# Optimization experiments

Measured on AMD Instinct MI355X. Metric: run time of the kernel, lower is better.

Reference implementation:

```python
import jax, jax.numpy as jnp
import numpy as np

IN_DIM = 128
OUT_DIM = 128
N_NODES = 50000
N_EDGES = 800000


def setup_inputs() -> dict:
    key = jax.random.key(0)
    ks = jax.random.split(key, 8)
    x = jax.random.normal(ks[0], (N_NODES, IN_DIM), dtype=jnp.float32)
    edge_index = jax.random.randint(ks[1], (2, N_EDGES), 0, N_NODES, dtype=jnp.int64)
    # SAGEConv params (PyG): lin_l applied to aggregated neighbors (has bias),
    # lin_r applied to root features (no bias).
    s = 1.0 / np.sqrt(IN_DIM)
    W_l = jax.random.uniform(ks[2], (IN_DIM, OUT_DIM), jnp.float32, -s, s)
    b_l = jax.random.uniform(ks[3], (OUT_DIM,), jnp.float32, -s, s)
    W_r = jax.random.uniform(ks[4], (IN_DIM, OUT_DIM), jnp.float32, -s, s)
    gamma = jnp.ones((OUT_DIM,), jnp.float32)
    beta = jnp.zeros((OUT_DIM,), jnp.float32)
    return {"x": x, "edge_index": edge_index, "W_l": W_l, "b_l": b_l,
            "W_r": W_r, "gamma": gamma, "beta": beta}


def reference(x, edge_index, W_l, b_l, W_r, gamma, beta):
    src, dst = edge_index[0], edge_index[1]
    # mean aggregation of source features at target nodes
    msg_sum = jax.ops.segment_sum(x[src], dst, num_segments=N_NODES)  # [N, in]
    cnt = jax.ops.segment_sum(jnp.ones((N_EDGES,), x.dtype), dst, num_segments=N_NODES)
    agg = msg_sum / jnp.maximum(cnt, 1.0)[:, None]
    # SAGEConv: lin_l(agg) + lin_r(x)
    out = agg @ W_l + b_l + x @ W_r  # [N, out]
    # LayerNorm over feature dim (eps=1e-5, torch default)
    mu = jnp.mean(out, axis=-1, keepdims=True)
    var = jnp.mean(jnp.square(out - mu), axis=-1, keepdims=True)
    out = (out - mu) * jax.lax.rsqrt(var + 1e-5) * gamma + beta
    # ReLU; dropout is identity in eval mode
    return jax.nn.relu(out)
```

## Files before the change

kernel.cpp:

```cpp
#include <hip/hip_runtime.h>

#define N_NODES 50000
#define N_EDGES 800000
#define DIM 128
#define M_PAD 50048

#define BNODES 64
#define NBUCK 782
#define SLACK 1280
#define EPB   4096
#define NBLKA ((N_EDGES + EPB - 1) / EPB)
#define SPLIT 2

#define M_TILE 32
#define MW 2

typedef __attribute__((ext_vector_type(8))) short bf16x8;
typedef __attribute__((ext_vector_type(4))) float f32x4;

#define WS_BUF_OFF 4096
#define WS_XH_OFF  (WS_BUF_OFF + (size_t)NBUCK * SLACK * 4)
#define WS_WT_OFF  (WS_XH_OFF + (size_t)M_PAD * DIM * 2)

static __device__ __forceinline__ unsigned short f2b(float f) {
    unsigned int x = __float_as_uint(f);
    x += 0x7fffu + ((x >> 16) & 1u);
    return (unsigned short)(x >> 16);
}
static __device__ __forceinline__ float blo(unsigned int v) {
    return __uint_as_float(v << 16);
}
static __device__ __forceinline__ float bhi(unsigned int v) {
    return __uint_as_float(v & 0xffff0000u);
}

#define CAST_BLOCKS 6250
#define WT_BLOCKS 64

__global__ __launch_bounds__(256) void prepA_kernel(
    const float* __restrict__ x,
    const float* __restrict__ Wl,
    const float* __restrict__ Wr,
    const int* __restrict__ src,
    const int* __restrict__ dst,
    unsigned short* __restrict__ xh,
    unsigned short* __restrict__ WhT,
    int* __restrict__ gcur,
    unsigned int* __restrict__ buf)
{
    __shared__ unsigned int img[EPB];
    __shared__ int hist[NBUCK];
    __shared__ int lbase[NBUCK];
    __shared__ int gbase[NBUCK];

    const int blk = blockIdx.x;
    const int tid = threadIdx.x;

    if (blk >= NBLKA) {
        int b = blk - NBLKA;
        if (b < CAST_BLOCKS) {
            int i = b * 256 + tid;
            float4 v = reinterpret_cast<const float4*>(x)[i];
            ushort4 h;
            h.x = f2b(v.x); h.y = f2b(v.y); h.z = f2b(v.z); h.w = f2b(v.w);
            reinterpret_cast<ushort4*>(xh)[i] = h;
        } else {
            int idx = (b - CAST_BLOCKS) * 256 + tid;
            int n = idx & 127;
            int k = idx >> 7;
            WhT[n * 256 + k]       = f2b(Wl[idx]);
            WhT[n * 256 + 128 + k] = f2b(Wr[idx]);
        }
        return;
    }

    const int e0 = blk * EPB;
    const int n = min(EPB, N_EDGES - e0);

    for (int i = tid; i < NBUCK; i += 256) hist[i] = 0;
    __syncthreads();
    for (int i = tid; i < n; i += 256)
        atomicAdd(&hist[dst[e0 + i] >> 6], 1);
    __syncthreads();
    if (tid < 64) {
        int c0 = tid * 13;
        int v[13];
        int s = 0;
        #pragma unroll
        for (int j = 0; j < 13; ++j) {
            int idx = c0 + j;
            v[j] = (idx < NBUCK) ? hist[idx] : 0;
            s += v[j];
        }
        int incl = s;
        #pragma unroll
        for (int d = 1; d < 64; d <<= 1) {
            int t = __shfl_up(incl, d, 64);
            if (tid >= d) incl += t;
        }
        int run = incl - s;
        #pragma unroll
        for (int j = 0; j < 13; ++j) {
            int idx = c0 + j;
            if (idx < NBUCK) lbase[idx] = run;
            run += v[j];
        }
    }
    __syncthreads();
    for (int i = tid; i < NBUCK; i += 256) {
        int c = hist[i];
        gbase[i] = i * SLACK + (c ? atomicAdd(&gcur[i], c) : 0);
        hist[i] = 0;
    }
    __syncthreads();
    for (int i = tid; i < n; i += 256) {
        int d = dst[e0 + i];
        int s = src[e0 + i];
        int b = d >> 6;
        int r = atomicAdd(&hist[b], 1);
        img[lbase[b] + r] = (unsigned int)s | ((unsigned int)d << 16);
    }
    __syncthreads();
    for (int i = tid; i < n; i += 256) {
        unsigned int v = img[i];
        int b = (int)(v >> 16) >> 6;
        int pos = gbase[b] + (i - lbase[b]);
        if (pos < (b + 1) * SLACK) buf[pos] = v;
    }
}

__global__ __launch_bounds__(256) void binBC_kernel(
    const unsigned int* __restrict__ buf,
    const int* __restrict__ gcur,
    const unsigned short* __restrict__ xh,
    const unsigned short* __restrict__ WhT,
    const float* __restrict__ bl,
    const float* __restrict__ gamma,
    const float* __restrict__ beta,
    float* __restrict__ out)
{
    __shared__ unsigned int ebuf[SLACK];
    __shared__ unsigned short csr[SLACK + 16];
    __shared__ int dhist[BNODES];
    __shared__ int dbase[BNODES];
    __shared__ int dcur[BNODES];
    __shared__ unsigned short aggh[M_TILE][DIM + 8];
    __shared__ float sRed[M_TILE][4][2];

    const int tid = threadIdx.x;
    const int w = tid >> 6;
    const int lane = tid & 63;
    const int r16 = lane & 15;
    const int kg = lane >> 4;
    const int b = blockIdx.x / SPLIT;
    const int half = blockIdx.x % SPLIT;
    const int rb = blockIdx.x * M_TILE;
    const int cnt = min(gcur[b], SLACK);
    const unsigned int* bp = buf + (size_t)b * SLACK;

    if (tid < BNODES) { dhist[tid] = 0; dcur[tid] = 0; }
    for (int i = tid; i < (SLACK + 16) / 2; i += 256)
        reinterpret_cast<unsigned int*>(csr)[i] = 0;
    for (int i = tid; i < cnt; i += 256) ebuf[i] = bp[i];
    __syncthreads();
    for (int i = tid; i < cnt; i += 256)
        atomicAdd(&dhist[(ebuf[i] >> 16) & 63], 1);
    __syncthreads();
    if (tid < 64) {
        int v = dhist[tid];
        int incl = v;
        #pragma unroll
        for (int d = 1; d < 64; d <<= 1) {
            int t = __shfl_up(incl, d, 64);
            if (tid >= d) incl += t;
        }
        dbase[tid] = incl - v;
    }
    __syncthreads();
    for (int i = tid; i < cnt; i += 256) {
        unsigned int v = ebuf[i];
        int d = (v >> 16) & 63;
        int r = atomicAdd(&dcur[d], 1);
        csr[dbase[d] + r] = (unsigned short)(v & 0xFFFFu);
    }
    __syncthreads();

    const unsigned int* xp = reinterpret_cast<const unsigned int*>(xh);
    for (int j = 0; j < M_TILE / 8; ++j) {
        int lnlA = w + 8 * j;
        int lnlB = lnlA + 4;
        int lnA = half * M_TILE + lnlA;
        int lnB = half * M_TILE + lnlB;
        int nodeA = b * BNODES + lnA;
        int nodeB = b * BNODES + lnB;
        int degA = (nodeA < N_NODES) ? dhist[lnA] : 0;
        int degB = (nodeB < N_NODES) ? dhist[lnB] : 0;
        int stA = dbase[lnA], stB = dbase[lnB];
        int dmA = max(degA - 1, 0), dmB = max(degB - 1, 0);
        float axA = 0.f, ayA = 0.f, axB = 0.f, ayB = 0.f;

        unsigned int vA[16], vB[16];
        #pragma unroll
        for (int t = 0; t < 16; ++t)
            vA[t] = xp[csr[stA + min(t, dmA)] * 64 + lane];
        #pragma unroll
        for (int t = 0; t < 16; ++t)
            vB[t] = xp[csr[stB + min(t, dmB)] * 64 + lane];
        #pragma unroll
        for (int t = 0; t < 16; ++t) {
            if (t < degA) { axA += blo(vA[t]); ayA += bhi(vA[t]); }
            if (t < degB) { axB += blo(vB[t]); ayB += bhi(vB[t]); }
        }
        for (int base = 16; base < degA; base += 8) {
            unsigned int u[8];
            #pragma unroll
            for (int t = 0; t < 8; ++t)
                u[t] = xp[csr[stA + min(base + t, dmA)] * 64 + lane];
            #pragma unroll
            for (int t = 0; t < 8; ++t)
                if (base + t < degA) { axA += blo(u[t]); ayA += bhi(u[t]); }
        }
        for (int base = 16; base < degB; base += 8) {
            unsigned int u[8];
            #pragma unroll
            for (int t = 0; t < 8; ++t)
                u[t] = xp[csr[stB + min(base + t, dmB)] * 64 + lane];
            #pragma unroll
            for (int t = 0; t < 8; ++t)
                if (base + t < degB) { axB += blo(u[t]); ayB += bhi(u[t]); }
        }
        float invA = 1.0f / (float)max(degA, 1);
        float invB = 1.0f / (float)max(degB, 1);
        unsigned int pkA = (unsigned int)f2b(axA * invA)
                         | ((unsigned int)f2b(ayA * invA) << 16);
        unsigned int pkB = (unsigned int)f2b(axB * invB)
                         | ((unsigned int)f2b(ayB * invB) << 16);
        *reinterpret_cast<unsigned int*>(&aggh[lnlA][lane * 2]) = pkA;
        *reinterpret_cast<unsigned int*>(&aggh[lnlB][lane * 2]) = pkB;
    }
    __syncthreads();

    f32x4 acc[MW][2];
    #pragma unroll
    for (int m = 0; m < MW; ++m)
        #pragma unroll
        for (int f = 0; f < 2; ++f)
            acc[m][f] = (f32x4){0.f, 0.f, 0.f, 0.f};

    #pragma unroll
    for (int kf = 0; kf < 8; ++kf) {
        bf16x8 a[MW];
        bf16x8 bfk[2];
        #pragma unroll
        for (int f = 0; f < 2; ++f)
            bfk[f] = *reinterpret_cast<const bf16x8*>(
                WhT + (w * 32 + f * 16 + r16) * 256 + kf * 32 + kg * 8);
        if (kf < 4) {
            #pragma unroll
            for (int m = 0; m < MW; ++m)
                a[m] = *reinterpret_cast<const bf16x8*>(
                    &aggh[m * 16 + r16][kf * 32 + kg * 8]);
        } else {
            #pragma unroll
            for (int m = 0; m < MW; ++m)
                a[m] = *reinterpret_cast<const bf16x8*>(
                    xh + (size_t)(rb + m * 16 + r16) * DIM + (kf - 4) * 32 + kg * 8);
        }
        #pragma unroll
        for (int m = 0; m < MW; ++m)
            #pragma unroll
            for (int f = 0; f < 2; ++f)
                acc[m][f] = __builtin_amdgcn_mfma_f32_16x16x32_bf16(
                    a[m], bfk[f], acc[m][f], 0, 0, 0);
    }

    float blv[2], gav[2], bev[2];
    #pragma unroll
    for (int f = 0; f < 2; ++f) {
        int col = w * 32 + f * 16 + r16;
        blv[f] = bl[col]; gav[f] = gamma[col]; bev[f] = beta[col];
    }
    #pragma unroll
    for (int m = 0; m < MW; ++m)
        #pragma unroll
        for (int r = 0; r < 4; ++r) {
            float v0 = acc[m][0][r] + blv[0];
            float v1 = acc[m][1][r] + blv[1];
            acc[m][0][r] = v0; acc[m][1][r] = v1;
            float s = v0 + v1;
            float q = v0 * v0 + v1 * v1;
            #pragma unroll
            for (int d = 1; d < 16; d <<= 1) {
                s += __shfl_xor(s, d, 16);
                q += __shfl_xor(q, d, 16);
            }
            if (r16 == 0) {
                sRed[m * 16 + kg * 4 + r][w][0] = s;
                sRed[m * 16 + kg * 4 + r][w][1] = q;
            }
        }
    __syncthreads();

    #pragma unroll
    for (int m = 0; m < MW; ++m)
        #pragma unroll
        for (int r = 0; r < 4; ++r) {
            int lr = m * 16 + kg * 4 + r;
            float S = sRed[lr][0][0] + sRed[lr][1][0] + sRed[lr][2][0] + sRed[lr][3][0];
            float Q = sRed[lr][0][1] + sRed[lr][1][1] + sRed[lr][2][1] + sRed[lr][3][1];
            float mean = S * (1.0f / 128.0f);
            float var = Q * (1.0f / 128.0f) - mean * mean;
            float rstd = rsqrtf(var + 1e-5f);
            int row = rb + lr;
            if (row < N_NODES) {
                #pragma unroll
                for (int f = 0; f < 2; ++f) {
                    float o = (acc[m][f][r] - mean) * rstd * gav[f] + bev[f];
                    out[(size_t)row * DIM + w * 32 + f * 16 + r16] = fmaxf(o, 0.f);
                }
            }
        }
}

extern "C" void kernel_launch(void* const* d_in, const int* in_sizes, int n_in,
                              void* d_out, int out_size, void* d_ws, size_t ws_size,
                              hipStream_t stream) {
    const float* x     = (const float*)d_in[0];
    const int*   ei    = (const int*)d_in[1];
    const float* Wl    = (const float*)d_in[2];
    const float* bl    = (const float*)d_in[3];
    const float* Wr    = (const float*)d_in[4];
    const float* gamma = (const float*)d_in[5];
    const float* beta  = (const float*)d_in[6];
    float* out = (float*)d_out;
    int*           gcur = (int*)d_ws;
    unsigned int*  buf  = (unsigned int*)((char*)d_ws + WS_BUF_OFF);
    unsigned short* xh  = (unsigned short*)((char*)d_ws + WS_XH_OFF);
    unsigned short* WhT = (unsigned short*)((char*)d_ws + WS_WT_OFF);

    const int* src = ei;
    const int* dst = ei + N_EDGES;

    (void)hipMemsetAsync(gcur, 0, 1024 * sizeof(int), stream);

    prepA_kernel<<<NBLKA + CAST_BLOCKS + WT_BLOCKS, 256, 0, stream>>>(
        x, Wl, Wr, src, dst, xh, WhT, gcur, buf);
    binBC_kernel<<<NBUCK * SPLIT, 256, 0, stream>>>(
        buf, gcur, xh, WhT, bl, gamma, beta, out);
}
```

Baseline: 78.45 us.

## Gather neighbor rows with 8-byte loads split across half-waves, four nodes per pass

Result: slower. 95.30 us (+21.5%).

```diff
diff --git a/kernel.cpp b/kernel.cpp
--- a/kernel.cpp
+++ b/kernel.cpp
@@ -17,6 +17,7 @@
 
 typedef __attribute__((ext_vector_type(8))) short bf16x8;
 typedef __attribute__((ext_vector_type(4))) float f32x4;
+typedef __attribute__((ext_vector_type(2))) unsigned int u32x2;
 
 #define WS_BUF_OFF 4096
 #define WS_XH_OFF  (WS_BUF_OFF + (size_t)NBUCK * SLACK * 4)
@@ -185,58 +186,78 @@
     }
     __syncthreads();
 
-    const unsigned int* xp = reinterpret_cast<const unsigned int*>(xh);
-    for (int j = 0; j < M_TILE / 8; ++j) {
-        int lnlA = w + 8 * j;
-        int lnlB = lnlA + 4;
-        int lnA = half * M_TILE + lnlA;
-        int lnB = half * M_TILE + lnlB;
-        int nodeA = b * BNODES + lnA;
-        int nodeB = b * BNODES + lnB;
-        int degA = (nodeA < N_NODES) ? dhist[lnA] : 0;
-        int degB = (nodeB < N_NODES) ? dhist[lnB] : 0;
-        int stA = dbase[lnA], stB = dbase[lnB];
-        int dmA = max(degA - 1, 0), dmB = max(degB - 1, 0);
-        float axA = 0.f, ayA = 0.f, axB = 0.f, ayB = 0.f;
-
-        unsigned int vA[16], vB[16];
-        #pragma unroll
-        for (int t = 0; t < 16; ++t)
-            vA[t] = xp[csr[stA + min(t, dmA)] * 64 + lane];
-        #pragma unroll
-        for (int t = 0; t < 16; ++t)
-            vB[t] = xp[csr[stB + min(t, dmB)] * 64 + lane];
-        #pragma unroll
-        for (int t = 0; t < 16; ++t) {
-            if (t < degA) { axA += blo(vA[t]); ayA += bhi(vA[t]); }
-            if (t < degB) { axB += blo(vB[t]); ayB += bhi(vB[t]); }
-        }
-        for (int base = 16; base < degA; base += 8) {
-            unsigned int u[8];
-            #pragma unroll
-            for (int t = 0; t < 8; ++t)
-                u[t] = xp[csr[stA + min(base + t, dmA)] * 64 + lane];
-            #pragma unroll
-            for (int t = 0; t < 8; ++t)
-                if (base + t < degA) { axA += blo(u[t]); ayA += bhi(u[t]); }
-        }
-        for (int base = 16; base < degB; base += 8) {
-            unsigned int u[8];
-            #pragma unroll
-            for (int t = 0; t < 8; ++t)
-                u[t] = xp[csr[stB + min(base + t, dmB)] * 64 + lane];
-            #pragma unroll
-            for (int t = 0; t < 8; ++t)
-                if (base + t < degB) { axB += blo(u[t]); ayB += bhi(u[t]); }
-        }
-        float invA = 1.0f / (float)max(degA, 1);
-        float invB = 1.0f / (float)max(degB, 1);
-        unsigned int pkA = (unsigned int)f2b(axA * invA)
-                         | ((unsigned int)f2b(ayA * invA) << 16);
-        unsigned int pkB = (unsigned int)f2b(axB * invB)
-                         | ((unsigned int)f2b(ayB * invB) << 16);
-        *reinterpret_cast<unsigned int*>(&aggh[lnlA][lane * 2]) = pkA;
-        *reinterpret_cast<unsigned int*>(&aggh[lnlB][lane * 2]) = pkB;
+    const char* xb = reinterpret_cast<const char*>(xh);
+    const int h2 = lane >> 5;
+    const int sub = lane & 31;
+    const unsigned loff = (unsigned)(sub * 8);
+
+    for (int q = 0; q < 2; ++q) {
+        int lnl[4], deg[4], st[4], dm[4];
+        #pragma unroll
+        for (int i = 0; i < 4; ++i) {
+            lnl[i] = w + 4 * i + 16 * q;
+            int ln = half * M_TILE + lnl[i];
+            int node = b * BNODES + ln;
+            deg[i] = (node < N_NODES) ? dhist[ln] : 0;
+            st[i] = dbase[ln];
+            dm[i] = max(deg[i] - 1, 0);
+        }
+        u32x2 vv[4][8];
+        #pragma unroll
+        for (int i = 0; i < 4; ++i)
+            #pragma unroll
+            for (int t = 0; t < 8; ++t) {
+                int e = t * 2 + h2;
+                unsigned off = (unsigned)csr[st[i] + min(e, dm[i])] * 256u + loff;
+                vv[i][t] = *reinterpret_cast<const u32x2*>(xb + off);
+            }
+        float a0[4], a1[4], a2[4], a3[4];
+        #pragma unroll
+        for (int i = 0; i < 4; ++i) { a0[i] = a1[i] = a2[i] = a3[i] = 0.f; }
+        #pragma unroll
+        for (int i = 0; i < 4; ++i)
+            #pragma unroll
+            for (int t = 0; t < 8; ++t) {
+                int e = t * 2 + h2;
+                if (e < deg[i]) {
+                    a0[i] += blo(vv[i][t].x); a1[i] += bhi(vv[i][t].x);
+                    a2[i] += blo(vv[i][t].y); a3[i] += bhi(vv[i][t].y);
+                }
+            }
+        #pragma unroll
+        for (int i = 0; i < 4; ++i) {
+            for (int base = 16; base < deg[i]; base += 8) {
+                u32x2 u[4];
+                #pragma unroll
+                for (int t = 0; t < 4; ++t) {
+                    int e = base + t * 2 + h2;
+                    unsigned off = (unsigned)csr[st[i] + min(e, dm[i])] * 256u + loff;
+                    u[t] = *reinterpret_cast<const u32x2*>(xb + off);
+                }
+                #pragma unroll
+                for (int t = 0; t < 4; ++t) {
+                    int e = base + t * 2 + h2;
+                    if (e < deg[i]) {
+                        a0[i] += blo(u[t].x); a1[i] += bhi(u[t].x);
+                        a2[i] += blo(u[t].y); a3[i] += bhi(u[t].y);
+                    }
+                }
+            }
+        }
+        #pragma unroll
+        for (int i = 0; i < 4; ++i) {
+            a0[i] += __shfl_xor(a0[i], 32);
+            a1[i] += __shfl_xor(a1[i], 32);
+            a2[i] += __shfl_xor(a2[i], 32);
+            a3[i] += __shfl_xor(a3[i], 32);
+            float inv = 1.0f / (float)max(deg[i], 1);
+            if (h2 == 0) {
+                u32x2 pk;
+                pk.x = (unsigned)f2b(a0[i] * inv) | ((unsigned)f2b(a1[i] * inv) << 16);
+                pk.y = (unsigned)f2b(a2[i] * inv) | ((unsigned)f2b(a3[i] * inv) << 16);
+                *reinterpret_cast<u32x2*>(&aggh[lnl[i]][sub * 4]) = pk;
+            }
+        }
     }
     __syncthreads();
 
```
